# Optimization experiments

Measured on AMD Instinct MI355X. Metric: run time of the kernel, lower is better.

The kernel has to match this reference:

```python
import jax, jax.numpy as jnp
import numpy as np

B, SQ, SK, D, H = 8, 1024, 1024, 1024, 16
DH = D // H  # attention head size = 64
LN_EPS = 1e-5


def _layer_norm(x, g, b):
    m = jnp.mean(x, axis=-1, keepdims=True)
    v = jnp.mean(jnp.square(x - m), axis=-1, keepdims=True)
    return (x - m) * jax.lax.rsqrt(v + LN_EPS) * g + b


def setup_inputs() -> dict:
    key = jax.random.key(0)
    ks = jax.random.split(key, 12)
    s = 0.02
    return {
        "hidden_states": jax.random.normal(ks[0], (B, SQ, D), jnp.float32),
        "context": jax.random.normal(ks[1], (B, SK, D), jnp.float32),
        "Wq": jax.random.normal(ks[2], (D, D), jnp.float32) * s,
        "bq": jnp.zeros((D,), jnp.float32),
        "Wk": jax.random.normal(ks[3], (D, D), jnp.float32) * s,
        "bk": jnp.zeros((D,), jnp.float32),
        "Wv": jax.random.normal(ks[4], (D, D), jnp.float32) * s,
        "bv": jnp.zeros((D,), jnp.float32),
        "Wobs": jax.random.normal(ks[5], (D, D), jnp.float32) * s,
        "bobs": jnp.zeros((D,), jnp.float32),
        "Wmat": jax.random.normal(ks[6], (D, D), jnp.float32) * s,
        "bmat": jnp.zeros((D,), jnp.float32),
        "ln_g": jnp.ones((D,), jnp.float32),
        "ln_b": jnp.zeros((D,), jnp.float32),
    }


def reference(hidden_states, context, Wq, bq, Wk, bk, Wv, bv,
              Wobs, bobs, Wmat, bmat, ln_g, ln_b):
    # QKV projections (torch Linear: x @ W.T + b)
    q = hidden_states @ Wq.T + bq            # [B, SQ, D]
    k = context @ Wk.T + bk                  # [B, SK, D]
    v = context @ Wv.T + bv                  # [B, SK, D]

    # ---- Guide_Block: single-head SDPA over full D, then linear->ReLU->LN ----
    # (dropout is identity in eval mode)
    score = jnp.einsum('bqd,bkd->bqk', q, k) / np.sqrt(D)   # [B, SQ, SK]
    attn = jax.nn.softmax(score, axis=-1)
    gctx = jnp.einsum('bqk,bkd->bqd', attn, v)              # [B, SQ, D]
    new_q = _layer_norm(jax.nn.relu(gctx @ Wobs.T + bobs), ln_g, ln_b)
    new_k = _layer_norm(jax.nn.relu(k @ Wmat.T + bmat), ln_g, ln_b)

    # ---- Multi-head attention with guided q/k and original v ----
    qh = new_q.reshape(B, SQ, H, DH).transpose(0, 2, 1, 3)  # [B, H, SQ, DH]
    kh = new_k.reshape(B, SK, H, DH).transpose(0, 2, 1, 3)
    vh = v.reshape(B, SK, H, DH).transpose(0, 2, 1, 3)
    scores = jnp.einsum('bhqd,bhkd->bhqk', qh, kh) / np.sqrt(DH)
    probs = jax.nn.softmax(scores, axis=-1)                 # attn dropout = identity (eval)
    out = jnp.einsum('bhqk,bhkd->bhqd', probs, vh)          # [B, H, SQ, DH]
    return out.transpose(0, 2, 1, 3).reshape(B, SQ, D)
```

## Files before the change

### kernel.cpp

```cpp
#include <hip/hip_runtime.h>
#include <hip/hip_bf16.h>

#define DEV __device__ __forceinline__

using bf16x8 = __attribute__((ext_vector_type(8))) short;
using f32x4  = __attribute__((ext_vector_type(4))) float;

#define MFMA16(a, b, c) __builtin_amdgcn_mfma_f32_16x16x32_bf16((a), (b), (c), 0, 0, 0)

#define GLOAD_LDS16(gp, lp)                                                        \
  __builtin_amdgcn_global_load_lds(                                               \
      (__attribute__((address_space(1))) unsigned int*)(gp),                      \
      (__attribute__((address_space(3))) unsigned int*)(lp), 16, 0, 0)

DEV float b2f(unsigned short u) {
  union { float f; unsigned u; } x; x.u = ((unsigned)u) << 16; return x.f;
}
DEV unsigned short f2b(float f) {
  union { float f; unsigned u; } x; x.f = f;
  unsigned r = x.u + 0x7FFFu + ((x.u >> 16) & 1u);
  return (unsigned short)(r >> 16);
}
DEV unsigned short f2b_trunc(float f) {
  union { float f; unsigned u; } x; x.f = f;
  return (unsigned short)(x.u >> 16);
}

__global__ __launch_bounds__(256) void detect_kernel(
    const unsigned short* __restrict__ hs, int* __restrict__ flag) {
  __shared__ int red[4];
  const int t = threadIdx.x;
  const ushort4* p = (const ushort4*)hs;
  int cnt = 0;
#pragma unroll
  for (int j = 0; j < 16; j++) {
    ushort4 u = p[j * 256 + t];
    cnt += (((u.x >> 7) & 0xFF) == 0xFF) + (((u.y >> 7) & 0xFF) == 0xFF) +
           (((u.z >> 7) & 0xFF) == 0xFF) + (((u.w >> 7) & 0xFF) == 0xFF);
  }
#pragma unroll
  for (int off = 32; off >= 1; off >>= 1) cnt += __shfl_xor(cnt, off, 64);
  if ((t & 63) == 0) red[t >> 6] = cnt;
  __syncthreads();
  if (t == 0) flag[0] = (red[0] + red[1] + red[2] + red[3] >= 4) ? 1 : 0;
}

__global__ __launch_bounds__(256) void convert2_kernel(
    const void* __restrict__ s0, const void* __restrict__ s1,
    unsigned short* __restrict__ d0, unsigned short* __restrict__ d1,
    const int* __restrict__ flag) {
  const int bid = blockIdx.x;
  const void* src;
  unsigned short* dst;
  long off;
  if (bid < 8192) { src = s0; dst = d0; off = (long)bid * 1024; }
  else            { src = s1; dst = d1; off = (long)(bid - 8192) * 1024; }
  const long i = off + threadIdx.x * 4;
  ushort4 o;
  if (*flag) {
    float4 f = ((const float4*)src)[i >> 2];
    o.x = f2b(f.x); o.y = f2b(f.y); o.z = f2b(f.z); o.w = f2b(f.w);
  } else {
    o = ((const ushort4*)src)[i >> 2];
  }
  ((ushort4*)dst)[i >> 2] = o;
}

__global__ __launch_bounds__(256) void convert_w_kernel(
    const void* __restrict__ s0, const void* __restrict__ s1,
    const void* __restrict__ s2, const void* __restrict__ s3,
    const void* __restrict__ s4, unsigned short* __restrict__ dst,
    const int* __restrict__ flag) {
  const void* srcs[5] = {s0, s1, s2, s3, s4};
  const void* src = srcs[blockIdx.y];
  unsigned short* d = dst + (long)blockIdx.y * 1048576;
  const int i = (blockIdx.x * 256 + threadIdx.x) * 4;
  ushort4 o;
  if (*flag) {
    float4 f = ((const float4*)src)[i >> 2];
    o.x = f2b(f.x); o.y = f2b(f.y); o.z = f2b(f.z); o.w = f2b(f.w);
  } else {
    o = ((const ushort4*)src)[i >> 2];
  }
  ((ushort4*)d)[i >> 2] = o;
}

__global__ __launch_bounds__(256) void convert_vec_kernel(
    const void* __restrict__ s0, const void* __restrict__ s1,
    const void* __restrict__ s2, const void* __restrict__ s3,
    const void* __restrict__ s4, const void* __restrict__ s5,
    const void* __restrict__ s6, unsigned short* __restrict__ dst,
    const int* __restrict__ flag) {
  const void* srcs[7] = {s0, s1, s2, s3, s4, s5, s6};
  const void* src = srcs[blockIdx.x];
  unsigned short* d = dst + blockIdx.x * 1024;
  const int i = threadIdx.x * 4;
  ushort4 o;
  if (*flag) {
    float4 f = ((const float4*)src)[i >> 2];
    o.x = f2b(f.x); o.y = f2b(f.y); o.z = f2b(f.z); o.w = f2b(f.w);
  } else {
    o = ((const ushort4*)src)[i >> 2];
  }
  ((ushort4*)d)[i >> 2] = o;
}

template <int RELU, int OUTBF16, int BIAS, int SPLIT>
__global__ __launch_bounds__(256, 2) void gemm_bt_kernel(
    const unsigned short* __restrict__ A, const unsigned short* __restrict__ B,
    const unsigned short* __restrict__ bias, void* __restrict__ Cv,
    void* __restrict__ Cv2, int M, int N, int K, long sA_, long sB_, long sC_,
    float scale) {
  __shared__ unsigned short sA[2][128 * 32];
  __shared__ unsigned short sB[2][128 * 32];
  const int t = threadIdx.x;
  const int wave = t >> 6, lane = t & 63;
  const int quad = lane >> 4, col = lane & 15;
  const int wm = wave >> 1, wn = wave & 1;
  const long zb = blockIdx.z;
  const unsigned short* Ab = A + zb * sA_ + (long)blockIdx.x * 128 * K;
  const unsigned short* Bb = B + zb * sB_ + (long)blockIdx.y * 128 * K;
  const int r0 = t >> 2;
  const int c0 = (t & 3) * 8;

  f32x4 zz = {0.f, 0.f, 0.f, 0.f};
  f32x4 acc[4][4];
#pragma unroll
  for (int i = 0; i < 4; i++)
#pragma unroll
    for (int j = 0; j < 4; j++) acc[i][j] = zz;

  for (int k0 = 0; k0 < K; k0 += 64) {
    __syncthreads();
#pragma unroll
    for (int p = 0; p < 2; p++) {
      GLOAD_LDS16(Ab + (long)r0 * K + k0 + p * 32 + c0,        &sA[p][t * 8]);
      GLOAD_LDS16(Ab + (long)(64 + r0) * K + k0 + p * 32 + c0, &sA[p][2048 + t * 8]);
      GLOAD_LDS16(Bb + (long)r0 * K + k0 + p * 32 + c0,        &sB[p][t * 8]);
      GLOAD_LDS16(Bb + (long)(64 + r0) * K + k0 + p * 32 + c0, &sB[p][2048 + t * 8]);
    }
    __syncthreads();
#pragma unroll
    for (int p = 0; p < 2; p++) {
      bf16x8 af[4], bfr[4];
#pragma unroll
      for (int mi = 0; mi < 4; mi++)
        af[mi] = *(const bf16x8*)&sA[p][(wm * 64 + mi * 16 + col) * 32 + quad * 8];
#pragma unroll
      for (int ni = 0; ni < 4; ni++)
        bfr[ni] = *(const bf16x8*)&sB[p][(wn * 64 + ni * 16 + col) * 32 + quad * 8];
#pragma unroll
      for (int mi = 0; mi < 4; mi++)
#pragma unroll
        for (int ni = 0; ni < 4; ni++)
          acc[mi][ni] = MFMA16(af[mi], bfr[ni], acc[mi][ni]);
    }
  }

  const int Rm = blockIdx.x * 128 + wm * 64;
  const int Cn = blockIdx.y * 128 + wn * 64;
  float bs[4];
#pragma unroll
  for (int ni = 0; ni < 4; ni++)
    bs[ni] = BIAS ? b2f(bias[Cn + ni * 16 + col]) : 0.f;

  unsigned short* Cb = (unsigned short*)Cv;
  int Nw = N, cadj = 0;
  if (SPLIT) {
    Nw = N >> 1;
    if (blockIdx.y >= (gridDim.y >> 1)) { Cb = (unsigned short*)Cv2; cadj = Nw; }
  }
#pragma unroll
  for (int mi = 0; mi < 4; mi++)
#pragma unroll
    for (int ni = 0; ni < 4; ni++)
#pragma unroll
      for (int r = 0; r < 4; r++) {
        int rr = Rm + mi * 16 + quad * 4 + r;
        int cc = Cn + ni * 16 + col;
        float v = acc[mi][ni][r] * scale + bs[ni];
        if (RELU) v = fmaxf(v, 0.f);
        if (OUTBF16)
          Cb[zb * sC_ + (long)rr * Nw + (cc - cadj)] = f2b(v);
        else
          ((float*)Cv)[zb * sC_ + (long)rr * N + cc] = v;
      }
}

__global__ __launch_bounds__(256) void softmax_kernel(
    const float* __restrict__ S, unsigned short* __restrict__ P) {
  __shared__ float red[8];
  const long row = blockIdx.x;
  const int t = threadIdx.x;
  const float4 v4 = ((const float4*)(S + row * 1024))[t];
  float x[4] = {v4.x, v4.y, v4.z, v4.w};
  float m = fmaxf(fmaxf(x[0], x[1]), fmaxf(x[2], x[3]));
#pragma unroll
  for (int off = 32; off >= 1; off >>= 1) m = fmaxf(m, __shfl_xor(m, off, 64));
  if ((t & 63) == 0) red[t >> 6] = m;
  __syncthreads();
  m = fmaxf(fmaxf(red[0], red[1]), fmaxf(red[2], red[3]));
  float e[4], s = 0.f;
#pragma unroll
  for (int i = 0; i < 4; i++) { e[i] = __expf(x[i] - m); s += e[i]; }
#pragma unroll
  for (int off = 32; off >= 1; off >>= 1) s += __shfl_xor(s, off, 64);
  __syncthreads();
  if ((t & 63) == 0) red[4 + (t >> 6)] = s;
  __syncthreads();
  s = red[4] + red[5] + red[6] + red[7];
  float inv = 1.f / s;
  ushort4 o;
  o.x = f2b(e[0] * inv); o.y = f2b(e[1] * inv);
  o.z = f2b(e[2] * inv); o.w = f2b(e[3] * inv);
  ((ushort4*)(P + row * 1024))[t] = o;
}

DEV float block_sum(float v, float* red, int t) {
#pragma unroll
  for (int off = 32; off >= 1; off >>= 1) v += __shfl_xor(v, off, 64);
  __syncthreads();
  if ((t & 63) == 0) red[t >> 6] = v;
  __syncthreads();
  return red[0] + red[1] + red[2] + red[3];
}

__global__ __launch_bounds__(256) void layernorm2_kernel(
    const unsigned short* __restrict__ X0, const unsigned short* __restrict__ X1,
    const unsigned short* __restrict__ G, const unsigned short* __restrict__ Bt,
    unsigned short* __restrict__ Y0, unsigned short* __restrict__ Y1) {
  __shared__ float red[4];
  const int bid = blockIdx.x;
  const unsigned short* X;
  unsigned short* Y;
  if (bid < 8192) { X = X0 + (long)bid * 1024; Y = Y0 + (long)bid * 1024; }
  else { X = X1 + (long)(bid - 8192) * 1024; Y = Y1 + (long)(bid - 8192) * 1024; }
  const int t = threadIdx.x;
  ushort4 u = ((const ushort4*)X)[t];
  float x[4] = {b2f(u.x), b2f(u.y), b2f(u.z), b2f(u.w)};
  float s = x[0] + x[1] + x[2] + x[3];
  float mean = block_sum(s, red, t) * (1.f / 1024.f);
  float d0 = x[0] - mean, d1 = x[1] - mean, d2 = x[2] - mean, d3 = x[3] - mean;
  float vs = d0 * d0 + d1 * d1 + d2 * d2 + d3 * d3;
  float var = block_sum(vs, red, t) * (1.f / 1024.f);
  float rs = rsqrtf(var + 1e-5f);
  ushort4 gu = ((const ushort4*)G)[t];
  ushort4 bu = ((const ushort4*)Bt)[t];
  ushort4 o;
  o.x = f2b(d0 * rs * b2f(gu.x) + b2f(bu.x));
  o.y = f2b(d1 * rs * b2f(gu.y) + b2f(bu.y));
  o.z = f2b(d2 * rs * b2f(gu.z) + b2f(bu.z));
  o.w = f2b(d3 * rs * b2f(gu.w) + b2f(bu.w));
  ((ushort4*)Y)[t] = o;
}

__global__ __launch_bounds__(256) void transpose_kernel(
    const unsigned short* __restrict__ V, unsigned short* __restrict__ VT) {
  __shared__ unsigned short tile[32][33];
  const int b = blockIdx.z;
  const int d0 = blockIdx.x * 32, sk0 = blockIdx.y * 32;
  const int tx = threadIdx.x & 31, ty = threadIdx.x >> 5;
#pragma unroll
  for (int i = 0; i < 32; i += 8)
    tile[ty + i][tx] = V[((long)(b * 1024 + sk0 + ty + i)) * 1024 + d0 + tx];
  __syncthreads();
#pragma unroll
  for (int i = 0; i < 32; i += 8)
    VT[((long)(b * 1024 + d0 + ty + i)) * 1024 + sk0 + tx] = tile[tx][ty + i];
}

__global__ __launch_bounds__(256, 2) void flash_mha_kernel(
    const unsigned short* __restrict__ Q, const unsigned short* __restrict__ K,
    const unsigned short* __restrict__ VT, void* __restrict__ O,
    const int* __restrict__ flag) {
  __shared__ unsigned short sK[2][2][32 * 32];
  __shared__ unsigned short sV[2][64 * 32];
  __shared__ unsigned short sP[4][32 * 32];
  const int t = threadIdx.x;
  const int wave = t >> 6, lane = t & 63;
  const int quad = lane >> 4, col = lane & 15;
  const int b = blockIdx.z, h = blockIdx.y;
  const int q0 = blockIdx.x * 128 + wave * 32;

  const int h2 = t >> 7, i7 = t & 127;
  const unsigned short* Ksrc =
      K + ((long)(b * 1024 + (i7 >> 2))) * 1024 + h * 64 + h2 * 32 + (i7 & 3) * 8;
  const unsigned short* Vsrc =
      VT + ((long)(b * 1024 + h * 64 + (t >> 2))) * 1024 + (t & 3) * 8;

  bf16x8 aq[2][2];
  {
    const unsigned short* qp =
        Q + ((long)(b * 1024 + q0 + col)) * 1024 + h * 64 + quad * 8;
    aq[0][0] = *(const bf16x8*)(qp);
    aq[0][1] = *(const bf16x8*)(qp + 32);
    aq[1][0] = *(const bf16x8*)(qp + 16 * 1024);
    aq[1][1] = *(const bf16x8*)(qp + 16 * 1024 + 32);
  }

  const f32x4 zz = {0.f, 0.f, 0.f, 0.f};
  f32x4 o[2][4], l[2];
#pragma unroll
  for (int mt = 0; mt < 2; mt++) {
    l[mt] = zz;
#pragma unroll
    for (int n = 0; n < 4; n++) o[mt][n] = zz;
  }
  bf16x8 ones;
#pragma unroll
  for (int i = 0; i < 8; i++) ones[i] = (short)0x3F80;

#define STAGE_KV(bi, kv0)                                             \
  {                                                                   \
    GLOAD_LDS16(Ksrc + (long)(kv0) * 1024, &sK[bi][h2][i7 * 8]);      \
    GLOAD_LDS16(Vsrc + (kv0), &sV[bi][t * 8]);                        \
  }

  STAGE_KV(0, 0);
  unsigned short* pw = &sP[wave][0];
  for (int kt = 0; kt < 32; kt++) {
    const int bi = kt & 1;
    __syncthreads();
    if (kt < 31) STAGE_KV(bi ^ 1, (kt + 1) * 32);

    bf16x8 kf[2][2];
#pragma unroll
    for (int nt = 0; nt < 2; nt++)
#pragma unroll
      for (int kh = 0; kh < 2; kh++)
        kf[nt][kh] = *(const bf16x8*)&sK[bi][kh][(nt * 16 + col) * 32 + quad * 8];
    f32x4 s[2][2];
#pragma unroll
    for (int mt = 0; mt < 2; mt++)
#pragma unroll
      for (int nt = 0; nt < 2; nt++) {
        s[mt][nt] = MFMA16(aq[mt][0], kf[nt][0], zz);
        s[mt][nt] = MFMA16(aq[mt][1], kf[nt][1], s[mt][nt]);
      }
#pragma unroll
    for (int mt = 0; mt < 2; mt++)
#pragma unroll
      for (int nt = 0; nt < 2; nt++)
#pragma unroll
        for (int r = 0; r < 4; r++) {
          float p = __expf(s[mt][nt][r] * 0.125f);
          pw[(mt * 16 + quad * 4 + r) * 32 + nt * 16 + col] = f2b_trunc(p);
        }
    __asm__ __volatile__("s_waitcnt lgkmcnt(0)" ::: "memory");
    bf16x8 ap[2];
#pragma unroll
    for (int mt = 0; mt < 2; mt++)
      ap[mt] = *(const bf16x8*)&pw[(mt * 16 + col) * 32 + quad * 8];
#pragma unroll
    for (int mt = 0; mt < 2; mt++) l[mt] = MFMA16(ap[mt], ones, l[mt]);
    bf16x8 vf[4];
#pragma unroll
    for (int n = 0; n < 4; n++)
      vf[n] = *(const bf16x8*)&sV[bi][(n * 16 + col) * 32 + quad * 8];
#pragma unroll
    for (int mt = 0; mt < 2; mt++)
#pragma unroll
      for (int n = 0; n < 4; n++) o[mt][n] = MFMA16(ap[mt], vf[n], o[mt][n]);
  }
#undef STAGE_KV

  const int f32o = *flag;
#pragma unroll
  for (int mt = 0; mt < 2; mt++)
#pragma unroll
    for (int r = 0; r < 4; r++) {
      float inv = 1.f / l[mt][r];
      const long base =
          ((long)(b * 1024 + q0 + mt * 16 + quad * 4 + r)) * 1024 + h * 64 + col;
      if (f32o) {
        float* Of = (float*)O;
#pragma unroll
        for (int n = 0; n < 4; n++) Of[base + n * 16] = o[mt][n][r] * inv;
      } else {
        unsigned short* Ou = (unsigned short*)O;
#pragma unroll
        for (int n = 0; n < 4; n++) Ou[base + n * 16] = f2b(o[mt][n][r] * inv);
      }
    }
}

extern "C" void kernel_launch(void* const* d_in, const int* in_sizes, int n_in,
                              void* d_out, int out_size, void* d_ws,
                              size_t ws_size, hipStream_t stream) {
  (void)in_sizes; (void)n_in; (void)out_size; (void)ws_size;
  const void* hs   = d_in[0];
  const void* ctx  = d_in[1];
  const void* Wq   = d_in[2];
  const void* bq   = d_in[3];
  const void* Wk   = d_in[4];
  const void* bk   = d_in[5];
  const void* Wv   = d_in[6];
  const void* bv   = d_in[7];
  const void* Wobs = d_in[8];
  const void* bobs = d_in[9];
  const void* Wmat = d_in[10];
  const void* bmat = d_in[11];
  const void* lng  = d_in[12];
  const void* lnb  = d_in[13];

  const long E = 8LL * 1024 * 1024;
  const long W1 = 1024L * 1024L;
  unsigned short* base = (unsigned short*)d_ws;
  unsigned short* hsb   = base;
  unsigned short* ctxb  = base + E;
  unsigned short* Wb    = base + 2 * E;
  unsigned short* Wqb   = Wb;
  unsigned short* Wkb   = Wb + W1;
  unsigned short* Wvb   = Wb + 2 * W1;
  unsigned short* Wobsb = Wb + 3 * W1;
  unsigned short* Wmatb = Wb + 4 * W1;
  unsigned short* vecs  = base + 2 * E + 5 * W1;
  unsigned short* bqb   = vecs;
  unsigned short* bkb   = vecs + 1024;
  unsigned short* bvb   = vecs + 2048;
  unsigned short* bobsb = vecs + 3072;
  unsigned short* bmatb = vecs + 4096;
  unsigned short* lngb  = vecs + 5120;
  unsigned short* lnbb  = vecs + 6144;
  int* flag = (int*)(vecs + 32768);
  unsigned short* q     = vecs + W1;
  unsigned short* k     = q + E;
  unsigned short* v     = k + E;
  unsigned short* vT    = v + E;
  float* scores = (float*)(vT + E);
  unsigned short* nq    = (unsigned short*)scores;
  unsigned short* newq  = ((unsigned short*)scores) + E;
  unsigned short* probs = hsb;
  unsigned short* gctx  = ctxb;
  unsigned short* nk    = v;
  unsigned short* newk  = q;

  dim3 blk(256);
  const long S1 = 1024L * 1024L;

  detect_kernel<<<dim3(1), blk, 0, stream>>>((const unsigned short*)hs, flag);
  convert2_kernel<<<dim3(16384), blk, 0, stream>>>(hs, ctx, hsb, ctxb, flag);
  convert_w_kernel<<<dim3(1024, 5), blk, 0, stream>>>(Wq, Wk, Wv, Wobs, Wmat, Wb, flag);
  convert_vec_kernel<<<dim3(7), blk, 0, stream>>>(bq, bk, bv, bobs, bmat, lng, lnb,
                                                  vecs, flag);

  gemm_bt_kernel<0, 1, 1, 0><<<dim3(64, 8, 1), blk, 0, stream>>>(
      hsb, Wqb, bqb, q, q, 8192, 1024, 1024, 0, 0, 0, 1.f);
  gemm_bt_kernel<0, 1, 1, 1><<<dim3(64, 16, 1), blk, 0, stream>>>(
      ctxb, Wkb, bkb, k, v, 8192, 2048, 1024, 0, 0, 0, 1.f);
  transpose_kernel<<<dim3(32, 32, 8), blk, 0, stream>>>(v, vT);
  gemm_bt_kernel<0, 0, 0, 0><<<dim3(8, 8, 8), blk, 0, stream>>>(
      q, k, nullptr, scores, scores, 1024, 1024, 1024, S1, S1, S1, 0.03125f);
  softmax_kernel<<<dim3(8192), blk, 0, stream>>>(scores, probs);
  gemm_bt_kernel<0, 1, 0, 0><<<dim3(8, 8, 8), blk, 0, stream>>>(
      probs, vT, nullptr, gctx, gctx, 1024, 1024, 1024, S1, S1, S1, 1.f);
  gemm_bt_kernel<1, 1, 1, 0><<<dim3(64, 8, 1), blk, 0, stream>>>(
      gctx, Wobsb, bobsb, nq, nq, 8192, 1024, 1024, 0, 0, 0, 1.f);
  gemm_bt_kernel<1, 1, 1, 0><<<dim3(64, 8, 1), blk, 0, stream>>>(
      k, Wmatb, bmatb, nk, nk, 8192, 1024, 1024, 0, 0, 0, 1.f);
  layernorm2_kernel<<<dim3(16384), blk, 0, stream>>>(nq, nk, lngb, lnbb, newq, newk);
  flash_mha_kernel<<<dim3(8, 16, 8), blk, 0, stream>>>(
      newq, newk, vT, d_out, flag);
}
```

Measured before the change: 405.6 us.

## Rewrite flash MHA with 32x32 MFMA, register-resident P, swizzled LDS, larger tiles

Rewrites the final multi-head attention kernel to use 32x32x16 bf16 MFMA with 64-query tiles per wave and 64-key tiles per iteration. Scores are computed transposed so exp'd probabilities stay in registers as the A operand, removing the LDS round-trip for P. The ones-MFMA row sum is replaced by scalar accumulation with a shuffle and LDS reduction. K/V tiles use XOR-swizzled LDS layout to avoid bank conflicts, and blocks are remapped so consecutive blocks share heads for cache reuse. This raises register pressure and halves the grid.

```diff
diff --git a/kernel.cpp b/kernel.cpp
--- a/kernel.cpp
+++ b/kernel.cpp
@@ -5,8 +5,10 @@
 
 using bf16x8 = __attribute__((ext_vector_type(8))) short;
 using f32x4  = __attribute__((ext_vector_type(4))) float;
+using f32x16 = __attribute__((ext_vector_type(16))) float;
 
 #define MFMA16(a, b, c) __builtin_amdgcn_mfma_f32_16x16x32_bf16((a), (b), (c), 0, 0, 0)
+#define MFMA32(a, b, c) __builtin_amdgcn_mfma_f32_32x32x16_bf16((a), (b), (c), 0, 0, 0)
 
 #define GLOAD_LDS16(gp, lp)                                                        \
   __builtin_amdgcn_global_load_lds(                                               \
@@ -273,113 +275,138 @@
     const unsigned short* __restrict__ Q, const unsigned short* __restrict__ K,
     const unsigned short* __restrict__ VT, void* __restrict__ O,
     const int* __restrict__ flag) {
-  __shared__ unsigned short sK[2][2][32 * 32];
-  __shared__ unsigned short sV[2][64 * 32];
-  __shared__ unsigned short sP[4][32 * 32];
+  __shared__ unsigned short sK[2][64 * 64];
+  __shared__ unsigned short sV[2][64 * 64];
+  __shared__ float lred[4][2][32];
   const int t = threadIdx.x;
   const int wave = t >> 6, lane = t & 63;
-  const int quad = lane >> 4, col = lane & 15;
-  const int b = blockIdx.z, h = blockIdx.y;
-  const int q0 = blockIdx.x * 128 + wave * 32;
-
-  const int h2 = t >> 7, i7 = t & 127;
-  const unsigned short* Ksrc =
-      K + ((long)(b * 1024 + (i7 >> 2))) * 1024 + h * 64 + h2 * 32 + (i7 & 3) * 8;
-  const unsigned short* Vsrc =
-      VT + ((long)(b * 1024 + h * 64 + (t >> 2))) * 1024 + (t & 3) * 8;
-
-  bf16x8 aq[2][2];
-  {
-    const unsigned short* qp =
-        Q + ((long)(b * 1024 + q0 + col)) * 1024 + h * 64 + quad * 8;
-    aq[0][0] = *(const bf16x8*)(qp);
-    aq[0][1] = *(const bf16x8*)(qp + 32);
-    aq[1][0] = *(const bf16x8*)(qp + 16 * 1024);
-    aq[1][1] = *(const bf16x8*)(qp + 16 * 1024 + 32);
-  }
-
-  const f32x4 zz = {0.f, 0.f, 0.f, 0.f};
-  f32x4 o[2][4], l[2];
-#pragma unroll
-  for (int mt = 0; mt < 2; mt++) {
-    l[mt] = zz;
-#pragma unroll
-    for (int n = 0; n < 4; n++) o[mt][n] = zz;
-  }
-  bf16x8 ones;
-#pragma unroll
-  for (int i = 0; i < 8; i++) ones[i] = (short)0x3F80;
-
-#define STAGE_KV(bi, kv0)                                             \
-  {                                                                   \
-    GLOAD_LDS16(Ksrc + (long)(kv0) * 1024, &sK[bi][h2][i7 * 8]);      \
-    GLOAD_LDS16(Vsrc + (kv0), &sV[bi][t * 8]);                        \
-  }
-
-  STAGE_KV(0, 0);
-  unsigned short* pw = &sP[wave][0];
-  for (int kt = 0; kt < 32; kt++) {
+  const int lr = lane & 31, lh = lane >> 5;
+
+  const int flat = blockIdx.x + (blockIdx.y << 2) + (blockIdx.z << 6);
+  const int w = (flat & 7) * 64 + (flat >> 3);
+  const int xq = w & 3, h = (w >> 2) & 15, b = w >> 6;
+  const int q0 = xq * 256 + wave * 64;
+
+  bf16x8 bq[2][4];
+#pragma unroll
+  for (int qt = 0; qt < 2; qt++)
+#pragma unroll
+    for (int d0 = 0; d0 < 4; d0++)
+      bq[qt][d0] = *(const bf16x8*)(Q +
+          ((long)(b * 1024 + q0 + qt * 32 + lr)) * 1024 + h * 64 + d0 * 16 + lh * 8);
+
+  const unsigned short* Ks[2];
+  const unsigned short* Vs[2];
+#pragma unroll
+  for (int j = 0; j < 2; j++) {
+    const int i = t + j * 256;
+    const int row = i >> 3;
+    const int c = ((i & 7) ^ (row & 7)) * 8;
+    const int prow = (row & ~12) | ((row & 4) << 1) | ((row & 8) >> 1);
+    Ks[j] = K + ((long)(b * 1024 + prow)) * 1024 + h * 64 + c;
+    Vs[j] = VT + ((long)(b * 1024 + h * 64 + row)) * 1024 + c;
+  }
+  const int lds0 = t * 8, lds1 = t * 8 + 2048;
+
+#define STAGE(bi, kv0)                                        \
+  {                                                           \
+    GLOAD_LDS16(Ks[0] + (long)(kv0) * 1024, &sK[bi][lds0]);   \
+    GLOAD_LDS16(Ks[1] + (long)(kv0) * 1024, &sK[bi][lds1]);   \
+    GLOAD_LDS16(Vs[0] + (kv0), &sV[bi][lds0]);                \
+    GLOAD_LDS16(Vs[1] + (kv0), &sV[bi][lds1]);                \
+  }
+
+  const f32x16 z16 = {0.f, 0.f, 0.f, 0.f, 0.f, 0.f, 0.f, 0.f,
+                      0.f, 0.f, 0.f, 0.f, 0.f, 0.f, 0.f, 0.f};
+  f32x16 o[2][2];
+#pragma unroll
+  for (int i = 0; i < 2; i++)
+#pragma unroll
+    for (int j = 0; j < 2; j++) o[i][j] = z16;
+  float lsum[2] = {0.f, 0.f};
+
+  STAGE(0, 0);
+  for (int kt = 0; kt < 16; kt++) {
     const int bi = kt & 1;
     __syncthreads();
-    if (kt < 31) STAGE_KV(bi ^ 1, (kt + 1) * 32);
-
-    bf16x8 kf[2][2];
-#pragma unroll
-    for (int nt = 0; nt < 2; nt++)
-#pragma unroll
-      for (int kh = 0; kh < 2; kh++)
-        kf[nt][kh] = *(const bf16x8*)&sK[bi][kh][(nt * 16 + col) * 32 + quad * 8];
-    f32x4 s[2][2];
-#pragma unroll
-    for (int mt = 0; mt < 2; mt++)
-#pragma unroll
-      for (int nt = 0; nt < 2; nt++) {
-        s[mt][nt] = MFMA16(aq[mt][0], kf[nt][0], zz);
-        s[mt][nt] = MFMA16(aq[mt][1], kf[nt][1], s[mt][nt]);
+    if (kt < 15) STAGE(bi ^ 1, (kt + 1) * 64);
+
+    f32x16 st[2][2];
+#pragma unroll
+    for (int i = 0; i < 2; i++)
+#pragma unroll
+      for (int j = 0; j < 2; j++) st[i][j] = z16;
+#pragma unroll
+    for (int kvt = 0; kvt < 2; kvt++) {
+      const int krow = kvt * 32 + lr;
+      const int kx = krow & 7;
+#pragma unroll
+      for (int d0 = 0; d0 < 4; d0++) {
+        const bf16x8 kf =
+            *(const bf16x8*)&sK[bi][krow * 64 + ((((d0 << 1) | lh) ^ kx) << 3)];
+        st[0][kvt] = MFMA32(kf, bq[0][d0], st[0][kvt]);
+        st[1][kvt] = MFMA32(kf, bq[1][d0], st[1][kvt]);
       }
-#pragma unroll
-    for (int mt = 0; mt < 2; mt++)
-#pragma unroll
-      for (int nt = 0; nt < 2; nt++)
-#pragma unroll
-        for (int r = 0; r < 4; r++) {
-          float p = __expf(s[mt][nt][r] * 0.125f);
-          pw[(mt * 16 + quad * 4 + r) * 32 + nt * 16 + col] = f2b_trunc(p);
+    }
+
+    bf16x8 pa[2][4];
+#pragma unroll
+    for (int qt = 0; qt < 2; qt++)
+#pragma unroll
+      for (int kvt = 0; kvt < 2; kvt++) {
+        float e[16];
+#pragma unroll
+        for (int r = 0; r < 16; r++) {
+          e[r] = exp2f(st[qt][kvt][r] * 0.18033688f);
+          lsum[qt] += e[r];
         }
-    __asm__ __volatile__("s_waitcnt lgkmcnt(0)" ::: "memory");
-    bf16x8 ap[2];
-#pragma unroll
-    for (int mt = 0; mt < 2; mt++)
-      ap[mt] = *(const bf16x8*)&pw[(mt * 16 + col) * 32 + quad * 8];
-#pragma unroll
-    for (int mt = 0; mt < 2; mt++) l[mt] = MFMA16(ap[mt], ones, l[mt]);
-    bf16x8 vf[4];
-#pragma unroll
-    for (int n = 0; n < 4; n++)
-      vf[n] = *(const bf16x8*)&sV[bi][(n * 16 + col) * 32 + quad * 8];
-#pragma unroll
-    for (int mt = 0; mt < 2; mt++)
-#pragma unroll
-      for (int n = 0; n < 4; n++) o[mt][n] = MFMA16(ap[mt], vf[n], o[mt][n]);
-  }
-#undef STAGE_KV
+        unsigned dw[8];
+#pragma unroll
+        for (int m = 0; m < 8; m++)
+          asm("v_cvt_pk_bf16_f32 %0, %1, %2"
+              : "=v"(dw[m]) : "v"(e[2 * m]), "v"(e[2 * m + 1]));
+        union { unsigned u[4]; bf16x8 v; } f0, f1;
+        f0.u[0] = dw[0]; f0.u[1] = dw[1]; f0.u[2] = dw[2]; f0.u[3] = dw[3];
+        f1.u[0] = dw[4]; f1.u[1] = dw[5]; f1.u[2] = dw[6]; f1.u[3] = dw[7];
+        pa[qt][kvt * 2] = f0.v;
+        pa[qt][kvt * 2 + 1] = f1.v;
+      }
+
+#pragma unroll
+    for (int kc = 0; kc < 4; kc++)
+#pragma unroll
+      for (int dht = 0; dht < 2; dht++) {
+        const int vrow = dht * 32 + lr;
+        const bf16x8 vf =
+            *(const bf16x8*)&sV[bi][vrow * 64 + ((((kc << 1) | lh) ^ (vrow & 7)) << 3)];
+        o[0][dht] = MFMA32(pa[0][kc], vf, o[0][dht]);
+        o[1][dht] = MFMA32(pa[1][kc], vf, o[1][dht]);
+      }
+  }
+#undef STAGE
+
+  float lt[2];
+#pragma unroll
+  for (int qt = 0; qt < 2; qt++)
+    lt[qt] = lsum[qt] + __shfl_xor(lsum[qt], 32, 64);
+  if (lane < 32) { lred[wave][0][lr] = lt[0]; lred[wave][1][lr] = lt[1]; }
+  __syncthreads();
 
   const int f32o = *flag;
 #pragma unroll
-  for (int mt = 0; mt < 2; mt++)
-#pragma unroll
-    for (int r = 0; r < 4; r++) {
-      float inv = 1.f / l[mt][r];
-      const long base =
-          ((long)(b * 1024 + q0 + mt * 16 + quad * 4 + r)) * 1024 + h * 64 + col;
+  for (int qt = 0; qt < 2; qt++)
+#pragma unroll
+    for (int r = 0; r < 16; r++) {
+      const int rowi = (lh << 2) + (r & 3) + ((r >> 2) << 3);
+      const float inv = 1.f / lred[wave][qt][rowi];
+      const long gr =
+          ((long)(b * 1024 + q0 + qt * 32 + rowi)) * 1024 + h * 64 + lr;
       if (f32o) {
-        float* Of = (float*)O;
-#pragma unroll
-        for (int n = 0; n < 4; n++) Of[base + n * 16] = o[mt][n][r] * inv;
+        ((float*)O)[gr] = o[qt][0][r] * inv;
+        ((float*)O)[gr + 32] = o[qt][1][r] * inv;
       } else {
-        unsigned short* Ou = (unsigned short*)O;
-#pragma unroll
-        for (int n = 0; n < 4; n++) Ou[base + n * 16] = f2b(o[mt][n][r] * inv);
+        ((unsigned short*)O)[gr] = f2b(o[qt][0][r] * inv);
+        ((unsigned short*)O)[gr + 32] = f2b(o[qt][1][r] * inv);
       }
     }
 }
@@ -459,6 +486,6 @@
   gemm_bt_kernel<1, 1, 1, 0><<<dim3(64, 8, 1), blk, 0, stream>>>(
       k, Wmatb, bmatb, nk, nk, 8192, 1024, 1024, 0, 0, 0, 1.f);
   layernorm2_kernel<<<dim3(16384), blk, 0, stream>>>(nq, nk, lngb, lnbb, newq, newk);
-  flash_mha_kernel<<<dim3(8, 16, 8), blk, 0, stream>>>(
+  flash_mha_kernel<<<dim3(4, 16, 8), blk, 0, stream>>>(
       newq, newk, vT, d_out, flag);
 }
```

Result: slower. 424.5 us (+4.7%).
